# Kernel tuning notes

Hardware: AMD Instinct MI355X
Metric: run time of the kernel (lower is better)

Reference implementation:

```python
import jax, jax.numpy as jnp
import numpy as np

N = 50000        # num_nodes
E = 800000       # num_edges
D_IN = 128
D_OUT = 128
BN_EPS = 1e-5    # torch BatchNorm1d default


def setup_inputs() -> dict:
    key = jax.random.key(0)
    ks = jax.random.split(key, 6)
    x = jax.random.normal(ks[0], (N, D_IN), dtype=jnp.float32)
    edge_index = jax.random.randint(ks[1], (2, E), 0, N, dtype=jnp.int64)
    eps = jnp.zeros((1,), dtype=jnp.float32)  # nn.Parameter(torch.tensor([0.0]))
    lim1 = 1.0 / np.sqrt(D_IN)
    lim2 = 1.0 / np.sqrt(D_OUT)
    W1 = jax.random.uniform(ks[2], (D_OUT, D_IN), jnp.float32, -lim1, lim1)
    b1 = jax.random.uniform(ks[3], (D_OUT,), jnp.float32, -lim1, lim1)
    W2 = jax.random.uniform(ks[4], (D_OUT, D_OUT), jnp.float32, -lim2, lim2)
    b2 = jax.random.uniform(ks[5], (D_OUT,), jnp.float32, -lim2, lim2)
    gamma1 = jnp.ones((D_OUT,), jnp.float32)
    beta1 = jnp.zeros((D_OUT,), jnp.float32)
    gamma2 = jnp.ones((D_OUT,), jnp.float32)
    beta2 = jnp.zeros((D_OUT,), jnp.float32)
    return {"x": x, "edge_index": edge_index, "eps": eps,
            "W1": W1, "b1": b1, "gamma1": gamma1, "beta1": beta1,
            "W2": W2, "b2": b2, "gamma2": gamma2, "beta2": beta2}


def _batch_norm(h, gamma, beta):
    # training-mode BatchNorm1d: biased batch variance, eps=1e-5
    mu = h.mean(axis=0)
    var = h.var(axis=0)
    return gamma * (h - mu) * jax.lax.rsqrt(var + BN_EPS) + beta


def reference(x, edge_index, eps, W1, b1, gamma1, beta1, W2, b2, gamma2, beta2):
    row, col = edge_index[0], edge_index[1]
    # agg[v] = sum_{(v,u) in edges} x[u]   (gather + scatter-add)
    agg = jax.ops.segment_sum(x[col], row, num_segments=N)  # [N, D_IN]
    out = (1.0 + eps) * x + agg                              # [N, D_IN]
    h = jax.nn.relu(_batch_norm(out @ W1.T + b1, gamma1, beta1))
    h = jax.nn.relu(_batch_norm(h @ W2.T + b2, gamma2, beta2))
    return h
```

## Files before the change

### kernel.cpp

```cpp
#include <hip/hip_runtime.h>

#define NN 50000
#define EE 800000
#define DD 128
#define BN_EPS 1e-5f
#define XCONV_B 3125
#define BIN_BLOCKS 200
#define BIN_EDGES 4000
#define NBUCK 1563
#define BCAP 1024
#define NREP 32
#define GEMM_B 782
#define LDA 136

typedef __attribute__((ext_vector_type(8))) short bf16x8;
typedef __attribute__((ext_vector_type(4))) float f32x4;
typedef __attribute__((ext_vector_type(8))) unsigned short u16x8;

__device__ inline unsigned short f2bf(float f) {
  unsigned int u = __float_as_uint(f);
  u = (u + 0x7fffu + ((u >> 16) & 1u)) >> 16;
  return (unsigned short)u;
}
__device__ inline float bf2f(unsigned short b) {
  return __uint_as_float(((unsigned int)b) << 16);
}


__global__ __launch_bounds__(256) void k_prep(const float* __restrict__ x,
                                              const float* __restrict__ W1,
                                              const float* __restrict__ W2,
                                              unsigned short* __restrict__ xb,
                                              unsigned short* __restrict__ W1b,
                                              unsigned short* __restrict__ W2b,
                                              int* __restrict__ bcur,
                                              float* __restrict__ reps) {
  const int b = blockIdx.x;
  const int t = threadIdx.x;
  if (b < XCONV_B) {
    const int gid = b * 256 + t;
    const float4 v0 = ((const float4*)x)[gid * 2];
    const float4 v1 = ((const float4*)x)[gid * 2 + 1];
    ushort4 o0, o1;
    o0.x = f2bf(v0.x); o0.y = f2bf(v0.y); o0.z = f2bf(v0.z); o0.w = f2bf(v0.w);
    o1.x = f2bf(v1.x); o1.y = f2bf(v1.y); o1.z = f2bf(v1.z); o1.w = f2bf(v1.w);
    ((ushort4*)xb)[gid * 2] = o0;
    ((ushort4*)xb)[gid * 2 + 1] = o1;
    if (gid < NBUCK) bcur[gid] = 0;
    if (gid < 4 * NREP * DD) reps[gid] = 0.0f;
  } else if (b < XCONV_B + 16) {
    const int gid = (b - XCONV_B) * 256 + t;
    const float4 v = ((const float4*)W1)[gid];
    ushort4 o;
    o.x = f2bf(v.x); o.y = f2bf(v.y); o.z = f2bf(v.z); o.w = f2bf(v.w);
    ((ushort4*)W1b)[gid] = o;
  } else {
    const int gid = (b - XCONV_B - 16) * 256 + t;
    const float4 v = ((const float4*)W2)[gid];
    ushort4 o;
    o.x = f2bf(v.x); o.y = f2bf(v.y); o.z = f2bf(v.z); o.w = f2bf(v.w);
    ((ushort4*)W2b)[gid] = o;
  }
}

__global__ __launch_bounds__(256) void k_bin0(const int* __restrict__ rows,
                                              const int* __restrict__ cols,
                                              int* __restrict__ bcur,
                                              unsigned int* __restrict__ bbuf) {
  __shared__ int hist[NBUCK];
  __shared__ int lbase[NBUCK];
  const int t = threadIdx.x;
  for (int i = t; i < NBUCK; i += 256) hist[i] = 0;
  __syncthreads();
  const int e0 = blockIdx.x * BIN_EDGES;
  int er[16], ec[16];
#pragma unroll
  for (int i = 0; i < 16; ++i) {
    const int idx = t + i * 256;
    if (idx < BIN_EDGES) {
      er[i] = rows[e0 + idx];
      ec[i] = cols[e0 + idx];
      atomicAdd(&hist[er[i] >> 5], 1);
    }
  }
  __syncthreads();
  for (int i = t; i < NBUCK; i += 256) {
    const int c = hist[i];
    lbase[i] = (c > 0) ? atomicAdd(&bcur[i], c) : 0;
    hist[i] = 0;
  }
  __syncthreads();
#pragma unroll
  for (int i = 0; i < 16; ++i) {
    const int idx = t + i * 256;
    if (idx < BIN_EDGES) {
      const int bk = er[i] >> 5;
      const int lp = lbase[bk] + atomicAdd(&hist[bk], 1);
      if (lp < BCAP)
        bbuf[(size_t)bk * BCAP + lp] =
            ((unsigned)(er[i] & 31) << 16) | (unsigned)ec[i];
    }
  }
}

__global__ __launch_bounds__(128) void k_aggemm1(
    const unsigned short* __restrict__ xb, const float* __restrict__ eps,
    const int* __restrict__ bcnt, const unsigned int* __restrict__ bbuf,
    const unsigned short* __restrict__ W, const float* __restrict__ bias,
    unsigned short* __restrict__ outb, float* __restrict__ sum1r,
    float* __restrict__ sumsq1r) {
  __shared__ unsigned short scols[BCAP];
  __shared__ unsigned short sA[32 * LDA];
  __shared__ int rcnt[32];
  __shared__ int roff[33];
  __shared__ int sscan[128];
  __shared__ float bsum[DD];
  __shared__ float bsq[DD];
  const int t = threadIdx.x;
  const int bk = blockIdx.x;
  const int wv = t >> 6;
  const int lane = t & 63;
  const int sub = lane >> 4;
  const int l16 = lane & 15;

  int n = bcnt[bk];
  n = n < BCAP ? n : BCAP;
  if (t < 32) rcnt[t] = 0;
  bsum[t] = 0.f;
  bsq[t] = 0.f;
  __syncthreads();

  unsigned int ent[8];
  int nl = 0;
  for (int i = t; i < n; i += 128) {
    const unsigned int e = bbuf[(size_t)bk * BCAP + i];
    ent[nl++] = e;
    atomicAdd(&rcnt[e >> 16], 1);
  }
  __syncthreads();
  sscan[t] = (t < 32) ? rcnt[t] : 0;
  __syncthreads();
#pragma unroll
  for (int off = 1; off < 32; off <<= 1) {
    const int v = (t >= off) ? sscan[t - off] : 0;
    __syncthreads();
    sscan[t] += v;
    __syncthreads();
  }
  if (t < 32) {
    roff[t] = sscan[t] - rcnt[t];
    rcnt[t] = 0;
  }
  if (t == 31) roff[32] = sscan[31];
  __syncthreads();
  for (int i = 0; i < nl; ++i) {
    const int r = ent[i] >> 16;
    const int pos = roff[r] + atomicAdd(&rcnt[r], 1);
    scols[pos] = (unsigned short)(ent[i] & 0xffffu);
  }
  __syncthreads();

  {
    const float s = 1.0f + eps[0];
    for (int r = wv; r < 32; r += 2) {
      const int v = bk * 32 + r;
      float acc[8];
#pragma unroll
      for (int j = 0; j < 8; ++j) acc[j] = 0.f;
      if (v < NN) {
        if (sub == 0) {
          const u16x8 a = *(const u16x8*)(xb + (size_t)v * DD + l16 * 8);
#pragma unroll
          for (int j = 0; j < 8; ++j) acc[j] = s * bf2f(a[j]);
        }
        const int beg = roff[r];
        const int end = roff[r + 1];
        int i = beg + sub;
        for (; i + 12 < end; i += 16) {
          const int u0 = scols[i];
          const int u1 = scols[i + 4];
          const int u2 = scols[i + 8];
          const int u3 = scols[i + 12];
          const u16x8 a = *(const u16x8*)(xb + (size_t)u0 * DD + l16 * 8);
          const u16x8 b = *(const u16x8*)(xb + (size_t)u1 * DD + l16 * 8);
          const u16x8 c = *(const u16x8*)(xb + (size_t)u2 * DD + l16 * 8);
          const u16x8 d = *(const u16x8*)(xb + (size_t)u3 * DD + l16 * 8);
#pragma unroll
          for (int j = 0; j < 8; ++j)
            acc[j] += (bf2f(a[j]) + bf2f(b[j])) + (bf2f(c[j]) + bf2f(d[j]));
        }
        for (; i + 4 < end; i += 8) {
          const int u0 = scols[i];
          const int u1 = scols[i + 4];
          const u16x8 a = *(const u16x8*)(xb + (size_t)u0 * DD + l16 * 8);
          const u16x8 b = *(const u16x8*)(xb + (size_t)u1 * DD + l16 * 8);
#pragma unroll
          for (int j = 0; j < 8; ++j) acc[j] += bf2f(a[j]) + bf2f(b[j]);
        }
        if (i < end) {
          const int u = scols[i];
          const u16x8 a = *(const u16x8*)(xb + (size_t)u * DD + l16 * 8);
#pragma unroll
          for (int j = 0; j < 8; ++j) acc[j] += bf2f(a[j]);
        }
      }
#pragma unroll
      for (int j = 0; j < 8; ++j) {
        acc[j] += __shfl_xor(acc[j], 16);
        acc[j] += __shfl_xor(acc[j], 32);
      }
      if (sub == 0) {
        u16x8 o;
#pragma unroll
        for (int j = 0; j < 8; ++j) o[j] = f2bf(acc[j]);
        *(u16x8*)(&sA[r * LDA + l16 * 8]) = o;
      }
    }
  }
  __syncthreads();

  f32x4 acc[8];
#pragma unroll
  for (int nn = 0; nn < 8; ++nn) acc[nn] = (f32x4){0.f, 0.f, 0.f, 0.f};
#pragma unroll
  for (int kk = 0; kk < 4; ++kk) {
    const bf16x8 af =
        *(const bf16x8*)(&sA[(wv * 16 + l16) * LDA + kk * 32 + sub * 8]);
#pragma unroll
    for (int nn = 0; nn < 8; ++nn) {
      const bf16x8 bf =
          *(const bf16x8*)(W + (size_t)(nn * 16 + l16) * DD + sub * 8 + kk * 32);
      acc[nn] = __builtin_amdgcn_mfma_f32_16x16x32_bf16(af, bf, acc[nn], 0, 0, 0);
    }
  }
  const int orow0 = bk * 32 + wv * 16 + sub * 4;
#pragma unroll
  for (int nn = 0; nn < 8; ++nn) {
    const int col = nn * 16 + l16;
    const float bv = bias[col];
    float sv = 0.f, qv = 0.f;
#pragma unroll
    for (int r = 0; r < 4; ++r) {
      const int row = orow0 + r;
      if (row < NN) {
        const float o = acc[nn][r] + bv;
        outb[(size_t)row * DD + col] = f2bf(o);
        sv += o; qv += o * o;
      }
    }
    sv += __shfl_xor(sv, 16); qv += __shfl_xor(qv, 16);
    sv += __shfl_xor(sv, 32); qv += __shfl_xor(qv, 32);
    if (sub == 0) { atomicAdd(&bsum[col], sv); atomicAdd(&bsq[col], qv); }
  }
  __syncthreads();
  {
    const int rep = (bk & (NREP - 1)) * DD;
    atomicAdd(&sum1r[rep + t], bsum[t]);
    atomicAdd(&sumsq1r[rep + t], bsq[t]);
  }
}

__global__ __launch_bounds__(256) void k_gemm2(const unsigned short* __restrict__ A,
                                               const float* __restrict__ sum1r,
                                               const float* __restrict__ sumsq1r,
                                               const float* __restrict__ gamma,
                                               const float* __restrict__ beta,
                                               const unsigned short* __restrict__ W,
                                               const float* __restrict__ bias,
                                               unsigned short* __restrict__ outb,
                                               float* __restrict__ sum2r,
                                               float* __restrict__ sumsq2r) {
  __shared__ float lsc[DD];
  __shared__ float lsh[DD];
  __shared__ float bsum[DD];
  __shared__ float bsq[DD];
  const int tid = threadIdx.x;
  const int wv = tid >> 6;
  const int lane = tid & 63;
  const int quad = lane >> 4;
  const int l16 = lane & 15;
  if (tid < DD) {
    float sm = 0.f, qm = 0.f;
#pragma unroll
    for (int r = 0; r < NREP; ++r) {
      sm += sum1r[r * DD + tid];
      qm += sumsq1r[r * DD + tid];
    }
    const float inv_n = 1.0f / (float)NN;
    const float mean = sm * inv_n;
    const float var = qm * inv_n - mean * mean;
    const float s = gamma[tid] * rsqrtf(var + BN_EPS);
    lsc[tid] = s;
    lsh[tid] = beta[tid] - mean * s;
    bsum[tid] = 0.f;
    bsq[tid] = 0.f;
  }
  __syncthreads();

  const int rowbase = blockIdx.x * 64 + wv * 16 + l16;
  const int arow = rowbase < NN ? rowbase : NN - 1;
  const unsigned short* aptr = A + (size_t)arow * DD + quad * 8;

  f32x4 acc[8];
#pragma unroll
  for (int n = 0; n < 8; ++n) acc[n] = (f32x4){0.f, 0.f, 0.f, 0.f};
#pragma unroll
  for (int kk = 0; kk < 4; ++kk) {
    const int kbase = kk * 32 + quad * 8;
    const u16x8 a = *(const u16x8*)(aptr + kk * 32);
    const float4 s0 = *(const float4*)&lsc[kbase];
    const float4 s1 = *(const float4*)&lsc[kbase + 4];
    const float4 h0 = *(const float4*)&lsh[kbase];
    const float4 h1 = *(const float4*)&lsh[kbase + 4];
    bf16x8 af;
    af[0] = (short)f2bf(fmaxf(fmaf(s0.x, bf2f(a[0]), h0.x), 0.f));
    af[1] = (short)f2bf(fmaxf(fmaf(s0.y, bf2f(a[1]), h0.y), 0.f));
    af[2] = (short)f2bf(fmaxf(fmaf(s0.z, bf2f(a[2]), h0.z), 0.f));
    af[3] = (short)f2bf(fmaxf(fmaf(s0.w, bf2f(a[3]), h0.w), 0.f));
    af[4] = (short)f2bf(fmaxf(fmaf(s1.x, bf2f(a[4]), h1.x), 0.f));
    af[5] = (short)f2bf(fmaxf(fmaf(s1.y, bf2f(a[5]), h1.y), 0.f));
    af[6] = (short)f2bf(fmaxf(fmaf(s1.z, bf2f(a[6]), h1.z), 0.f));
    af[7] = (short)f2bf(fmaxf(fmaf(s1.w, bf2f(a[7]), h1.w), 0.f));
#pragma unroll
    for (int n = 0; n < 8; ++n) {
      const bf16x8 bf =
          *(const bf16x8*)(W + (size_t)(n * 16 + l16) * DD + kbase);
      acc[n] = __builtin_amdgcn_mfma_f32_16x16x32_bf16(af, bf, acc[n], 0, 0, 0);
    }
  }
  const int orow0 = blockIdx.x * 64 + wv * 16 + quad * 4;
#pragma unroll
  for (int n = 0; n < 8; ++n) {
    const int col = n * 16 + l16;
    const float bv = bias[col];
    float sv = 0.f, qv = 0.f;
#pragma unroll
    for (int r = 0; r < 4; ++r) {
      const int row = orow0 + r;
      if (row < NN) {
        const float o = acc[n][r] + bv;
        outb[(size_t)row * DD + col] = f2bf(o);
        sv += o; qv += o * o;
      }
    }
    sv += __shfl_xor(sv, 16); qv += __shfl_xor(qv, 16);
    sv += __shfl_xor(sv, 32); qv += __shfl_xor(qv, 32);
    if (quad == 0) { atomicAdd(&bsum[col], sv); atomicAdd(&bsq[col], qv); }
  }
  __syncthreads();
  if (tid < DD) {
    const int rep = (blockIdx.x & (NREP - 1)) * DD;
    atomicAdd(&sum2r[rep + tid], bsum[tid]);
    atomicAdd(&sumsq2r[rep + tid], bsq[tid]);
  }
}

__global__ void k_bnstats2(const float* __restrict__ sum2r,
                           const float* __restrict__ sumsq2r,
                           const float* __restrict__ gamma,
                           const float* __restrict__ beta,
                           float* __restrict__ scale,
                           float* __restrict__ shift) {
  const int c = threadIdx.x;
  float sm = 0.f, qm = 0.f;
#pragma unroll
  for (int r = 0; r < NREP; ++r) {
    sm += sum2r[r * DD + c];
    qm += sumsq2r[r * DD + c];
  }
  const float inv_n = 1.0f / (float)NN;
  const float mean = sm * inv_n;
  const float var = qm * inv_n - mean * mean;
  const float sc = gamma[c] * rsqrtf(var + BN_EPS);
  scale[c] = sc;
  shift[c] = beta[c] - mean * sc;
}

__global__ __launch_bounds__(256) void k_bnrelu(const unsigned short* __restrict__ in,
                                                const float* __restrict__ scale,
                                                const float* __restrict__ shift,
                                                float* __restrict__ out) {
  __shared__ float lsc[DD];
  __shared__ float lsh[DD];
  const int t = threadIdx.x;
  if (t < DD) {
    lsc[t] = scale[t];
    lsh[t] = shift[t];
  }
  __syncthreads();
  const int gid = blockIdx.x * 256 + t;
  const int c = (gid & 15) * 8;
  const u16x8 a = ((const u16x8*)in)[gid];
  const float4 sc0 = *(const float4*)&lsc[c];
  const float4 sc1 = *(const float4*)&lsc[c + 4];
  const float4 sh0 = *(const float4*)&lsh[c];
  const float4 sh1 = *(const float4*)&lsh[c + 4];
  float4 o0, o1;
  o0.x = fmaxf(fmaf(sc0.x, bf2f(a[0]), sh0.x), 0.f);
  o0.y = fmaxf(fmaf(sc0.y, bf2f(a[1]), sh0.y), 0.f);
  o0.z = fmaxf(fmaf(sc0.z, bf2f(a[2]), sh0.z), 0.f);
  o0.w = fmaxf(fmaf(sc0.w, bf2f(a[3]), sh0.w), 0.f);
  o1.x = fmaxf(fmaf(sc1.x, bf2f(a[4]), sh1.x), 0.f);
  o1.y = fmaxf(fmaf(sc1.y, bf2f(a[5]), sh1.y), 0.f);
  o1.z = fmaxf(fmaf(sc1.z, bf2f(a[6]), sh1.z), 0.f);
  o1.w = fmaxf(fmaf(sc1.w, bf2f(a[7]), sh1.w), 0.f);
  ((float4*)out)[gid * 2] = o0;
  ((float4*)out)[gid * 2 + 1] = o1;
}

extern "C" void kernel_launch(void* const* d_in, const int* in_sizes, int n_in,
                              void* d_out, int out_size, void* d_ws, size_t ws_size,
                              hipStream_t stream) {
  const float* x = (const float*)d_in[0];
  const int* ei = (const int*)d_in[1];
  const float* eps = (const float*)d_in[2];
  const float* W1 = (const float*)d_in[3];
  const float* b1 = (const float*)d_in[4];
  const float* g1 = (const float*)d_in[5];
  const float* be1 = (const float*)d_in[6];
  const float* W2 = (const float*)d_in[7];
  const float* b2 = (const float*)d_in[8];
  const float* g2 = (const float*)d_in[9];
  const float* be2 = (const float*)d_in[10];
  float* out = (float*)d_out;

  const int* rows = ei;
  const int* cols = ei + EE;

  int* bcur = (int*)d_out;
  unsigned short* xb = (unsigned short*)d_out + 2000000;
  unsigned int* bbuf = (unsigned int*)((char*)d_out + 16800000);
  unsigned short* W1b = (unsigned short*)d_out + 11640000;
  unsigned short* W2b = (unsigned short*)d_out + 11680000;
  float* reps = (float*)d_out + 5875000;
  float* sum1r = reps;
  float* sumsq1r = reps + NREP * DD;
  float* sum2r = reps + 2 * NREP * DD;
  float* sumsq2r = reps + 3 * NREP * DD;

  unsigned short* h1b = (unsigned short*)d_ws;
  unsigned short* h2b = h1b + (size_t)NN * DD;
  float* stats = (float*)(h1b + (size_t)2 * NN * DD);
  float* scale2 = stats + 0;
  float* shift2 = stats + 128;

  k_prep<<<XCONV_B + 32, 256, 0, stream>>>(x, W1, W2, xb, W1b, W2b, bcur, reps);
  k_bin0<<<BIN_BLOCKS, 256, 0, stream>>>(rows, cols, bcur, bbuf);
  k_aggemm1<<<NBUCK, 128, 0, stream>>>(xb, eps, bcur, bbuf, W1b, b1, h1b,
                                       sum1r, sumsq1r);
  k_gemm2<<<GEMM_B, 256, 0, stream>>>(h1b, sum1r, sumsq1r, g1, be1, W2b, b2,
                                      h2b, sum2r, sumsq2r);
  k_bnstats2<<<1, 128, 0, stream>>>(sum2r, sumsq2r, g2, be2, scale2, shift2);
  k_bnrelu<<<(NN * DD / 8) / 256, 256, 0, stream>>>(h2b, scale2, shift2, out);
}
```

Before: 202.4 us.

## Widen aggregation-GEMM blocks to four waves and fold BN2 stats into gemm2

The fused aggregate+GEMM1 kernel now runs 256 threads (four waves) per bucket. Rows are split across four waves and the MFMA tile across a 2x2 wave grid, and the 32-entry prefix scan becomes a wave shuffle scan instead of a multi-barrier shared-memory scan. The separate single-block BN2 statistics kernel is removed: the last gemm2 block, found through an atomic done counter zeroed in prep, reduces the replicated sums and writes scale and shift. This saves one kernel launch and raises per-block parallelism, at the cost of extra fences and a last-block serialization tail.

```diff
diff --git a/kernel.cpp b/kernel.cpp
--- a/kernel.cpp
+++ b/kernel.cpp
@@ -46,7 +46,7 @@
     o1.x = f2bf(v1.x); o1.y = f2bf(v1.y); o1.z = f2bf(v1.z); o1.w = f2bf(v1.w);
     ((ushort4*)xb)[gid * 2] = o0;
     ((ushort4*)xb)[gid * 2 + 1] = o1;
-    if (gid < NBUCK) bcur[gid] = 0;
+    if (gid <= NBUCK) bcur[gid] = 0;
     if (gid < 4 * NREP * DD) reps[gid] = 0.0f;
   } else if (b < XCONV_B + 16) {
     const int gid = (b - XCONV_B) * 256 + t;
@@ -103,7 +103,7 @@
   }
 }
 
-__global__ __launch_bounds__(128) void k_aggemm1(
+__global__ __launch_bounds__(256) void k_aggemm1(
     const unsigned short* __restrict__ xb, const float* __restrict__ eps,
     const int* __restrict__ bcnt, const unsigned int* __restrict__ bbuf,
     const unsigned short* __restrict__ W, const float* __restrict__ bias,
@@ -113,7 +113,6 @@
   __shared__ unsigned short sA[32 * LDA];
   __shared__ int rcnt[32];
   __shared__ int roff[33];
-  __shared__ int sscan[128];
   __shared__ float bsum[DD];
   __shared__ float bsq[DD];
   const int t = threadIdx.x;
@@ -126,32 +125,28 @@
   int n = bcnt[bk];
   n = n < BCAP ? n : BCAP;
   if (t < 32) rcnt[t] = 0;
-  bsum[t] = 0.f;
-  bsq[t] = 0.f;
-  __syncthreads();
-
-  unsigned int ent[8];
+  if (t < DD) { bsum[t] = 0.f; bsq[t] = 0.f; }
+  __syncthreads();
+
+  unsigned int ent[4];
   int nl = 0;
-  for (int i = t; i < n; i += 128) {
+  for (int i = t; i < n; i += 256) {
     const unsigned int e = bbuf[(size_t)bk * BCAP + i];
     ent[nl++] = e;
     atomicAdd(&rcnt[e >> 16], 1);
   }
   __syncthreads();
-  sscan[t] = (t < 32) ? rcnt[t] : 0;
-  __syncthreads();
-#pragma unroll
-  for (int off = 1; off < 32; off <<= 1) {
-    const int v = (t >= off) ? sscan[t - off] : 0;
-    __syncthreads();
-    sscan[t] += v;
-    __syncthreads();
-  }
-  if (t < 32) {
-    roff[t] = sscan[t] - rcnt[t];
-    rcnt[t] = 0;
-  }
-  if (t == 31) roff[32] = sscan[31];
+  if (t < 64) {
+    int v = (t < 32) ? rcnt[t] : 0;
+#pragma unroll
+    for (int off = 1; off < 32; off <<= 1) {
+      const int u = __shfl_up(v, off);
+      if (lane >= off) v += u;
+    }
+    if (t < 32) roff[t] = v - rcnt[t];
+    if (t == 31) roff[32] = v;
+    if (t < 32) rcnt[t] = 0;
+  }
   __syncthreads();
   for (int i = 0; i < nl; ++i) {
     const int r = ent[i] >> 16;
@@ -162,7 +157,7 @@
 
   {
     const float s = 1.0f + eps[0];
-    for (int r = wv; r < 32; r += 2) {
+    for (int r = wv; r < 32; r += 4) {
       const int v = bk * 32 + r;
       float acc[8];
 #pragma unroll
@@ -219,24 +214,26 @@
   }
   __syncthreads();
 
-  f32x4 acc[8];
-#pragma unroll
-  for (int nn = 0; nn < 8; ++nn) acc[nn] = (f32x4){0.f, 0.f, 0.f, 0.f};
+  const int wr = wv & 1;
+  const int wc = wv >> 1;
+  f32x4 acc[4];
+#pragma unroll
+  for (int nn = 0; nn < 4; ++nn) acc[nn] = (f32x4){0.f, 0.f, 0.f, 0.f};
 #pragma unroll
   for (int kk = 0; kk < 4; ++kk) {
     const bf16x8 af =
-        *(const bf16x8*)(&sA[(wv * 16 + l16) * LDA + kk * 32 + sub * 8]);
-#pragma unroll
-    for (int nn = 0; nn < 8; ++nn) {
-      const bf16x8 bf =
-          *(const bf16x8*)(W + (size_t)(nn * 16 + l16) * DD + sub * 8 + kk * 32);
+        *(const bf16x8*)(&sA[(wr * 16 + l16) * LDA + kk * 32 + sub * 8]);
+#pragma unroll
+    for (int nn = 0; nn < 4; ++nn) {
+      const bf16x8 bf = *(const bf16x8*)(
+          W + (size_t)(wc * 64 + nn * 16 + l16) * DD + sub * 8 + kk * 32);
       acc[nn] = __builtin_amdgcn_mfma_f32_16x16x32_bf16(af, bf, acc[nn], 0, 0, 0);
     }
   }
-  const int orow0 = bk * 32 + wv * 16 + sub * 4;
-#pragma unroll
-  for (int nn = 0; nn < 8; ++nn) {
-    const int col = nn * 16 + l16;
+  const int orow0 = bk * 32 + wr * 16 + sub * 4;
+#pragma unroll
+  for (int nn = 0; nn < 4; ++nn) {
+    const int col = wc * 64 + nn * 16 + l16;
     const float bv = bias[col];
     float sv = 0.f, qv = 0.f;
 #pragma unroll
@@ -253,7 +250,7 @@
     if (sub == 0) { atomicAdd(&bsum[col], sv); atomicAdd(&bsq[col], qv); }
   }
   __syncthreads();
-  {
+  if (t < DD) {
     const int rep = (bk & (NREP - 1)) * DD;
     atomicAdd(&sum1r[rep + t], bsum[t]);
     atomicAdd(&sumsq1r[rep + t], bsq[t]);
@@ -269,7 +266,12 @@
                                                const float* __restrict__ bias,
                                                unsigned short* __restrict__ outb,
                                                float* __restrict__ sum2r,
-                                               float* __restrict__ sumsq2r) {
+                                               float* __restrict__ sumsq2r,
+                                               const float* __restrict__ gamma2,
+                                               const float* __restrict__ beta2,
+                                               float* __restrict__ scale2,
+                                               float* __restrict__ shift2,
+                                               int* __restrict__ done) {
   __shared__ float lsc[DD];
   __shared__ float lsh[DD];
   __shared__ float bsum[DD];
@@ -353,27 +355,30 @@
     atomicAdd(&sum2r[rep + tid], bsum[tid]);
     atomicAdd(&sumsq2r[rep + tid], bsq[tid]);
   }
-}
-
-__global__ void k_bnstats2(const float* __restrict__ sum2r,
-                           const float* __restrict__ sumsq2r,
-                           const float* __restrict__ gamma,
-                           const float* __restrict__ beta,
-                           float* __restrict__ scale,
-                           float* __restrict__ shift) {
-  const int c = threadIdx.x;
-  float sm = 0.f, qm = 0.f;
-#pragma unroll
-  for (int r = 0; r < NREP; ++r) {
-    sm += sum2r[r * DD + c];
-    qm += sumsq2r[r * DD + c];
-  }
-  const float inv_n = 1.0f / (float)NN;
-  const float mean = sm * inv_n;
-  const float var = qm * inv_n - mean * mean;
-  const float sc = gamma[c] * rsqrtf(var + BN_EPS);
-  scale[c] = sc;
-  shift[c] = beta[c] - mean * sc;
+
+  __threadfence();
+  __shared__ int amlast;
+  if (tid == 0) amlast = (atomicAdd(done, 1) == GEMM_B - 1) ? 1 : 0;
+  __syncthreads();
+  if (amlast) {
+    __threadfence();
+    if (tid < DD) {
+      float sm = 0.f, qm = 0.f;
+#pragma unroll
+      for (int r = 0; r < NREP; ++r) {
+        sm += __hip_atomic_load(&sum2r[r * DD + tid], __ATOMIC_RELAXED,
+                                __HIP_MEMORY_SCOPE_AGENT);
+        qm += __hip_atomic_load(&sumsq2r[r * DD + tid], __ATOMIC_RELAXED,
+                                __HIP_MEMORY_SCOPE_AGENT);
+      }
+      const float inv_n = 1.0f / (float)NN;
+      const float mean = sm * inv_n;
+      const float var = qm * inv_n - mean * mean;
+      const float sc = gamma2[tid] * rsqrtf(var + BN_EPS);
+      scale2[tid] = sc;
+      shift2[tid] = beta2[tid] - mean * sc;
+    }
+  }
 }
 
 __global__ __launch_bounds__(256) void k_bnrelu(const unsigned short* __restrict__ in,
@@ -437,6 +442,7 @@
   float* sumsq1r = reps + NREP * DD;
   float* sum2r = reps + 2 * NREP * DD;
   float* sumsq2r = reps + 3 * NREP * DD;
+  int* done = bcur + NBUCK;
 
   unsigned short* h1b = (unsigned short*)d_ws;
   unsigned short* h2b = h1b + (size_t)NN * DD;
@@ -446,10 +452,10 @@
 
   k_prep<<<XCONV_B + 32, 256, 0, stream>>>(x, W1, W2, xb, W1b, W2b, bcur, reps);
   k_bin0<<<BIN_BLOCKS, 256, 0, stream>>>(rows, cols, bcur, bbuf);
-  k_aggemm1<<<NBUCK, 128, 0, stream>>>(xb, eps, bcur, bbuf, W1b, b1, h1b,
+  k_aggemm1<<<NBUCK, 256, 0, stream>>>(xb, eps, bcur, bbuf, W1b, b1, h1b,
                                        sum1r, sumsq1r);
   k_gemm2<<<GEMM_B, 256, 0, stream>>>(h1b, sum1r, sumsq1r, g1, be1, W2b, b2,
-                                      h2b, sum2r, sumsq2r);
-  k_bnstats2<<<1, 128, 0, stream>>>(sum2r, sumsq2r, g2, be2, scale2, shift2);
+                                      h2b, sum2r, sumsq2r, g2, be2,
+                                      scale2, shift2, done);
   k_bnrelu<<<(NN * DD / 8) / 256, 256, 0, stream>>>(h2b, scale2, shift2, out);
 }
```

Result: slower. 264.6 us (+30.7%).

## Split aggregation by feature quarter and fuse both MLP layers with grid-wide barriers

Applied to the files above, without the earlier changes.

Stores x in bf16 as four 32-column planes and runs aggregation as four passes, one per plane, over 16-row buckets. Each pass gathers narrower rows, which improves cache locality for the random neighbour gathers. Both GEMMs, both batch-norm statistic reductions and the final BN+ReLU move into one persistent kernel of 391 blocks. That kernel uses last-block election plus spin-wait barriers on global flags, which removes the h1/h2 round trips and three kernel launches. The cost is that it only works if all blocks are co-resident, and the aggregated result now makes an extra trip through memory.

```diff
diff --git a/kernel.cpp b/kernel.cpp
--- a/kernel.cpp
+++ b/kernel.cpp
@@ -7,10 +7,11 @@
 #define XCONV_B 3125
 #define BIN_BLOCKS 200
 #define BIN_EDGES 4000
-#define NBUCK 1563
-#define BCAP 1024
+#define NBUCK 3125
+#define BROWS 16
+#define BCAP 512
 #define NREP 32
-#define GEMM_B 782
+#define MLP_B 391
 #define LDA 136
 
 typedef __attribute__((ext_vector_type(8))) short bf16x8;
@@ -25,16 +26,23 @@
 __device__ inline float bf2f(unsigned short b) {
   return __uint_as_float(((unsigned int)b) << 16);
 }
+__device__ inline float ldw(const float* p) {
+  return __hip_atomic_load(p, __ATOMIC_RELAXED, __HIP_MEMORY_SCOPE_AGENT);
+}
+__device__ inline void stw(float* p, float v) {
+  __hip_atomic_store(p, v, __ATOMIC_RELAXED, __HIP_MEMORY_SCOPE_AGENT);
+}
 
 
 __global__ __launch_bounds__(256) void k_prep(const float* __restrict__ x,
                                               const float* __restrict__ W1,
                                               const float* __restrict__ W2,
-                                              unsigned short* __restrict__ xb,
+                                              unsigned short* __restrict__ xq,
                                               unsigned short* __restrict__ W1b,
                                               unsigned short* __restrict__ W2b,
                                               int* __restrict__ bcur,
-                                              float* __restrict__ reps) {
+                                              float* __restrict__ reps,
+                                              int* __restrict__ syncw) {
   const int b = blockIdx.x;
   const int t = threadIdx.x;
   if (b < XCONV_B) {
@@ -44,10 +52,14 @@
     ushort4 o0, o1;
     o0.x = f2bf(v0.x); o0.y = f2bf(v0.y); o0.z = f2bf(v0.z); o0.w = f2bf(v0.w);
     o1.x = f2bf(v1.x); o1.y = f2bf(v1.y); o1.z = f2bf(v1.z); o1.w = f2bf(v1.w);
-    ((ushort4*)xb)[gid * 2] = o0;
-    ((ushort4*)xb)[gid * 2 + 1] = o1;
+    const int node = gid >> 4;
+    const int c0 = (gid & 15) * 8;
+    const size_t dst = (size_t)(c0 >> 5) * (NN * 32) + node * 32 + (c0 & 31);
+    *(ushort4*)(xq + dst) = o0;
+    *(ushort4*)(xq + dst + 4) = o1;
     if (gid < NBUCK) bcur[gid] = 0;
     if (gid < 4 * NREP * DD) reps[gid] = 0.0f;
+    if (gid < 4) syncw[gid] = 0;
   } else if (b < XCONV_B + 16) {
     const int gid = (b - XCONV_B) * 256 + t;
     const float4 v = ((const float4*)W1)[gid];
@@ -80,7 +92,7 @@
     if (idx < BIN_EDGES) {
       er[i] = rows[e0 + idx];
       ec[i] = cols[e0 + idx];
-      atomicAdd(&hist[er[i] >> 5], 1);
+      atomicAdd(&hist[er[i] >> 4], 1);
     }
   }
   __syncthreads();
@@ -94,43 +106,33 @@
   for (int i = 0; i < 16; ++i) {
     const int idx = t + i * 256;
     if (idx < BIN_EDGES) {
-      const int bk = er[i] >> 5;
+      const int bk = er[i] >> 4;
       const int lp = lbase[bk] + atomicAdd(&hist[bk], 1);
       if (lp < BCAP)
         bbuf[(size_t)bk * BCAP + lp] =
-            ((unsigned)(er[i] & 31) << 16) | (unsigned)ec[i];
-    }
-  }
-}
-
-__global__ __launch_bounds__(128) void k_aggemm1(
-    const unsigned short* __restrict__ xb, const float* __restrict__ eps,
+            ((unsigned)(er[i] & 15) << 16) | (unsigned)ec[i];
+    }
+  }
+}
+
+__global__ __launch_bounds__(128) void k_agg(
+    const unsigned short* __restrict__ xq, const float* __restrict__ eps,
     const int* __restrict__ bcnt, const unsigned int* __restrict__ bbuf,
-    const unsigned short* __restrict__ W, const float* __restrict__ bias,
-    unsigned short* __restrict__ outb, float* __restrict__ sum1r,
-    float* __restrict__ sumsq1r) {
+    unsigned short* __restrict__ aggb) {
   __shared__ unsigned short scols[BCAP];
-  __shared__ unsigned short sA[32 * LDA];
-  __shared__ int rcnt[32];
-  __shared__ int roff[33];
-  __shared__ int sscan[128];
-  __shared__ float bsum[DD];
-  __shared__ float bsq[DD];
+  __shared__ int rcnt[BROWS];
+  __shared__ int roff[BROWS + 1];
   const int t = threadIdx.x;
-  const int bk = blockIdx.x;
-  const int wv = t >> 6;
-  const int lane = t & 63;
-  const int sub = lane >> 4;
-  const int l16 = lane & 15;
+  const int id = blockIdx.x;
+  const int q = id / NBUCK;
+  const int bk = id - q * NBUCK;
 
   int n = bcnt[bk];
   n = n < BCAP ? n : BCAP;
-  if (t < 32) rcnt[t] = 0;
-  bsum[t] = 0.f;
-  bsq[t] = 0.f;
-  __syncthreads();
-
-  unsigned int ent[8];
+  if (t < BROWS) rcnt[t] = 0;
+  __syncthreads();
+
+  unsigned int ent[4];
   int nl = 0;
   for (int i = t; i < n; i += 128) {
     const unsigned int e = bbuf[(size_t)bk * BCAP + i];
@@ -138,20 +140,17 @@
     atomicAdd(&rcnt[e >> 16], 1);
   }
   __syncthreads();
-  sscan[t] = (t < 32) ? rcnt[t] : 0;
-  __syncthreads();
-#pragma unroll
-  for (int off = 1; off < 32; off <<= 1) {
-    const int v = (t >= off) ? sscan[t - off] : 0;
-    __syncthreads();
-    sscan[t] += v;
-    __syncthreads();
-  }
-  if (t < 32) {
-    roff[t] = sscan[t] - rcnt[t];
+  if (t < BROWS) {
+    int v = rcnt[t];
+#pragma unroll
+    for (int off = 1; off < BROWS; off <<= 1) {
+      const int u = __shfl_up(v, off);
+      if (t >= off) v += u;
+    }
+    roff[t] = v - rcnt[t];
+    if (t == BROWS - 1) roff[BROWS] = v;
     rcnt[t] = 0;
   }
-  if (t == 31) roff[32] = sscan[31];
   __syncthreads();
   for (int i = 0; i < nl; ++i) {
     const int r = ent[i] >> 16;
@@ -160,252 +159,277 @@
   }
   __syncthreads();
 
-  {
-    const float s = 1.0f + eps[0];
-    for (int r = wv; r < 32; r += 2) {
-      const int v = bk * 32 + r;
-      float acc[8];
-#pragma unroll
-      for (int j = 0; j < 8; ++j) acc[j] = 0.f;
-      if (v < NN) {
-        if (sub == 0) {
-          const u16x8 a = *(const u16x8*)(xb + (size_t)v * DD + l16 * 8);
-#pragma unroll
-          for (int j = 0; j < 8; ++j) acc[j] = s * bf2f(a[j]);
-        }
-        const int beg = roff[r];
-        const int end = roff[r + 1];
-        int i = beg + sub;
-        for (; i + 12 < end; i += 16) {
-          const int u0 = scols[i];
-          const int u1 = scols[i + 4];
-          const int u2 = scols[i + 8];
-          const int u3 = scols[i + 12];
-          const u16x8 a = *(const u16x8*)(xb + (size_t)u0 * DD + l16 * 8);
-          const u16x8 b = *(const u16x8*)(xb + (size_t)u1 * DD + l16 * 8);
-          const u16x8 c = *(const u16x8*)(xb + (size_t)u2 * DD + l16 * 8);
-          const u16x8 d = *(const u16x8*)(xb + (size_t)u3 * DD + l16 * 8);
-#pragma unroll
-          for (int j = 0; j < 8; ++j)
-            acc[j] += (bf2f(a[j]) + bf2f(b[j])) + (bf2f(c[j]) + bf2f(d[j]));
-        }
-        for (; i + 4 < end; i += 8) {
-          const int u0 = scols[i];
-          const int u1 = scols[i + 4];
-          const u16x8 a = *(const u16x8*)(xb + (size_t)u0 * DD + l16 * 8);
-          const u16x8 b = *(const u16x8*)(xb + (size_t)u1 * DD + l16 * 8);
-#pragma unroll
-          for (int j = 0; j < 8; ++j) acc[j] += bf2f(a[j]) + bf2f(b[j]);
-        }
-        if (i < end) {
-          const int u = scols[i];
-          const u16x8 a = *(const u16x8*)(xb + (size_t)u * DD + l16 * 8);
-#pragma unroll
-          for (int j = 0; j < 8; ++j) acc[j] += bf2f(a[j]);
-        }
-      }
-#pragma unroll
-      for (int j = 0; j < 8; ++j) {
-        acc[j] += __shfl_xor(acc[j], 16);
-        acc[j] += __shfl_xor(acc[j], 32);
-      }
-      if (sub == 0) {
-        u16x8 o;
-#pragma unroll
-        for (int j = 0; j < 8; ++j) o[j] = f2bf(acc[j]);
-        *(u16x8*)(&sA[r * LDA + l16 * 8]) = o;
-      }
-    }
-  }
-  __syncthreads();
-
-  f32x4 acc[8];
-#pragma unroll
-  for (int nn = 0; nn < 8; ++nn) acc[nn] = (f32x4){0.f, 0.f, 0.f, 0.f};
-#pragma unroll
-  for (int kk = 0; kk < 4; ++kk) {
-    const bf16x8 af =
-        *(const bf16x8*)(&sA[(wv * 16 + l16) * LDA + kk * 32 + sub * 8]);
-#pragma unroll
-    for (int nn = 0; nn < 8; ++nn) {
-      const bf16x8 bf =
-          *(const bf16x8*)(W + (size_t)(nn * 16 + l16) * DD + sub * 8 + kk * 32);
-      acc[nn] = __builtin_amdgcn_mfma_f32_16x16x32_bf16(af, bf, acc[nn], 0, 0, 0);
-    }
-  }
-  const int orow0 = bk * 32 + wv * 16 + sub * 4;
-#pragma unroll
-  for (int nn = 0; nn < 8; ++nn) {
-    const int col = nn * 16 + l16;
-    const float bv = bias[col];
-    float sv = 0.f, qv = 0.f;
-#pragma unroll
-    for (int r = 0; r < 4; ++r) {
-      const int row = orow0 + r;
-      if (row < NN) {
-        const float o = acc[nn][r] + bv;
-        outb[(size_t)row * DD + col] = f2bf(o);
-        sv += o; qv += o * o;
-      }
-    }
-    sv += __shfl_xor(sv, 16); qv += __shfl_xor(qv, 16);
-    sv += __shfl_xor(sv, 32); qv += __shfl_xor(qv, 32);
-    if (sub == 0) { atomicAdd(&bsum[col], sv); atomicAdd(&bsq[col], qv); }
-  }
-  __syncthreads();
-  {
-    const int rep = (bk & (NREP - 1)) * DD;
-    atomicAdd(&sum1r[rep + t], bsum[t]);
-    atomicAdd(&sumsq1r[rep + t], bsq[t]);
-  }
-}
-
-__global__ __launch_bounds__(256) void k_gemm2(const unsigned short* __restrict__ A,
-                                               const float* __restrict__ sum1r,
-                                               const float* __restrict__ sumsq1r,
-                                               const float* __restrict__ gamma,
-                                               const float* __restrict__ beta,
-                                               const unsigned short* __restrict__ W,
-                                               const float* __restrict__ bias,
-                                               unsigned short* __restrict__ outb,
-                                               float* __restrict__ sum2r,
-                                               float* __restrict__ sumsq2r) {
+  const int g = t >> 3;
+  const int l8 = t & 3 | ((t & 7) & ~3);
+  const unsigned short* xqq = xq + (size_t)q * (NN * 32);
+  const float s = 1.0f + eps[0];
+  const int v = bk * BROWS + g;
+  const ushort4 sv4 = *(const ushort4*)(xqq + (size_t)v * 32 + (t & 7) * 4);
+  float a0 = s * bf2f(sv4.x);
+  float a1 = s * bf2f(sv4.y);
+  float a2 = s * bf2f(sv4.z);
+  float a3 = s * bf2f(sv4.w);
+  int i = roff[g];
+  const int E = roff[g + 1];
+  const int lo = (t & 7) * 4;
+  for (; i + 3 < E; i += 4) {
+    const int u0 = scols[i], u1 = scols[i + 1];
+    const int u2 = scols[i + 2], u3 = scols[i + 3];
+    const ushort4 p0 = *(const ushort4*)(xqq + (size_t)u0 * 32 + lo);
+    const ushort4 p1 = *(const ushort4*)(xqq + (size_t)u1 * 32 + lo);
+    const ushort4 p2 = *(const ushort4*)(xqq + (size_t)u2 * 32 + lo);
+    const ushort4 p3 = *(const ushort4*)(xqq + (size_t)u3 * 32 + lo);
+    a0 += (bf2f(p0.x) + bf2f(p1.x)) + (bf2f(p2.x) + bf2f(p3.x));
+    a1 += (bf2f(p0.y) + bf2f(p1.y)) + (bf2f(p2.y) + bf2f(p3.y));
+    a2 += (bf2f(p0.z) + bf2f(p1.z)) + (bf2f(p2.z) + bf2f(p3.z));
+    a3 += (bf2f(p0.w) + bf2f(p1.w)) + (bf2f(p2.w) + bf2f(p3.w));
+  }
+  for (; i + 1 < E; i += 2) {
+    const int u0 = scols[i], u1 = scols[i + 1];
+    const ushort4 p0 = *(const ushort4*)(xqq + (size_t)u0 * 32 + lo);
+    const ushort4 p1 = *(const ushort4*)(xqq + (size_t)u1 * 32 + lo);
+    a0 += bf2f(p0.x) + bf2f(p1.x);
+    a1 += bf2f(p0.y) + bf2f(p1.y);
+    a2 += bf2f(p0.z) + bf2f(p1.z);
+    a3 += bf2f(p0.w) + bf2f(p1.w);
+  }
+  if (i < E) {
+    const int u0 = scols[i];
+    const ushort4 p0 = *(const ushort4*)(xqq + (size_t)u0 * 32 + lo);
+    a0 += bf2f(p0.x);
+    a1 += bf2f(p0.y);
+    a2 += bf2f(p0.z);
+    a3 += bf2f(p0.w);
+  }
+  ushort4 o;
+  o.x = f2bf(a0); o.y = f2bf(a1); o.z = f2bf(a2); o.w = f2bf(a3);
+  *(ushort4*)(aggb + (size_t)v * DD + q * 32 + lo) = o;
+}
+
+__global__ __launch_bounds__(256, 2) void k_mlp(
+    const unsigned short* __restrict__ aggb, float* __restrict__ sum1r,
+    float* __restrict__ sumsq1r, const float* __restrict__ g1,
+    const float* __restrict__ be1, const unsigned short* __restrict__ W1b,
+    const float* __restrict__ b1, const unsigned short* __restrict__ W2b,
+    const float* __restrict__ b2, float* __restrict__ sum2r,
+    float* __restrict__ sumsq2r, const float* __restrict__ g2,
+    const float* __restrict__ be2, float* __restrict__ scale1,
+    float* __restrict__ shift1, float* __restrict__ scale2,
+    float* __restrict__ shift2, int* __restrict__ syncw,
+    float* __restrict__ out) {
+  __shared__ unsigned short sT[128 * LDA];
   __shared__ float lsc[DD];
   __shared__ float lsh[DD];
-  __shared__ float bsum[DD];
-  __shared__ float bsq[DD];
+  __shared__ int amlast;
   const int tid = threadIdx.x;
+  const int bk = blockIdx.x;
   const int wv = tid >> 6;
   const int lane = tid & 63;
   const int quad = lane >> 4;
   const int l16 = lane & 15;
+  const int rowq = bk * 128 + wv * 32 + quad * 4;
+
+#pragma unroll
+  for (int it = 0; it < 8; ++it) {
+    const int idx = it * 256 + tid;
+    const int row = idx >> 4, seg = idx & 15;
+    int grow = bk * 128 + row;
+    grow = grow < NN ? grow : NN - 1;
+    *(u16x8*)&sT[row * LDA + seg * 8] =
+        *(const u16x8*)(aggb + (size_t)grow * DD + seg * 8);
+  }
+  __syncthreads();
+
+  f32x4 acc[2][8];
+#pragma unroll
+  for (int m = 0; m < 2; ++m)
+#pragma unroll
+    for (int n = 0; n < 8; ++n) acc[m][n] = (f32x4){0.f, 0.f, 0.f, 0.f};
+#pragma unroll
+  for (int kk = 0; kk < 4; ++kk) {
+    const bf16x8 a0 =
+        *(const bf16x8*)&sT[(wv * 32 + l16) * LDA + kk * 32 + quad * 8];
+    const bf16x8 a1 =
+        *(const bf16x8*)&sT[(wv * 32 + 16 + l16) * LDA + kk * 32 + quad * 8];
+#pragma unroll
+    for (int n = 0; n < 8; ++n) {
+      const bf16x8 bf = *(const bf16x8*)(W1b + (size_t)(n * 16 + l16) * DD +
+                                         kk * 32 + quad * 8);
+      acc[0][n] = __builtin_amdgcn_mfma_f32_16x16x32_bf16(a0, bf, acc[0][n], 0, 0, 0);
+      acc[1][n] = __builtin_amdgcn_mfma_f32_16x16x32_bf16(a1, bf, acc[1][n], 0, 0, 0);
+    }
+  }
+#pragma unroll
+  for (int n = 0; n < 8; ++n) {
+    const int col = n * 16 + l16;
+    const float bv = b1[col];
+    float sv = 0.f, qv = 0.f;
+#pragma unroll
+    for (int m = 0; m < 2; ++m)
+#pragma unroll
+      for (int r = 0; r < 4; ++r) {
+        const float o = acc[m][n][r] + bv;
+        acc[m][n][r] = o;
+        if (rowq + m * 16 + r < NN) { sv += o; qv += o * o; }
+      }
+    sv += __shfl_xor(sv, 16); qv += __shfl_xor(qv, 16);
+    sv += __shfl_xor(sv, 32); qv += __shfl_xor(qv, 32);
+    if (quad == 0) {
+      const int rep = (bk & (NREP - 1)) * DD;
+      atomicAdd(&sum1r[rep + col], sv);
+      atomicAdd(&sumsq1r[rep + col], qv);
+    }
+  }
+  __syncthreads();
+#pragma unroll
+  for (int m = 0; m < 2; ++m)
+#pragma unroll
+    for (int n = 0; n < 8; ++n)
+#pragma unroll
+      for (int r = 0; r < 4; ++r)
+        sT[(wv * 32 + m * 16 + quad * 4 + r) * LDA + n * 16 + l16] =
+            f2bf(acc[m][n][r]);
+
+  if (tid == 0) amlast = (atomicAdd(&syncw[0], 1) == MLP_B - 1) ? 1 : 0;
+  __syncthreads();
+  if (amlast) {
+    if (tid < DD) {
+      float sm = 0.f, qm = 0.f;
+#pragma unroll
+      for (int r = 0; r < NREP; ++r) {
+        sm += ldw(&sum1r[r * DD + tid]);
+        qm += ldw(&sumsq1r[r * DD + tid]);
+      }
+      const float inv_n = 1.0f / (float)NN;
+      const float mean = sm * inv_n;
+      const float var = qm * inv_n - mean * mean;
+      const float sc = g1[tid] * rsqrtf(var + BN_EPS);
+      stw(&scale1[tid], sc);
+      stw(&shift1[tid], be1[tid] - mean * sc);
+    }
+    __syncthreads();
+    if (tid == 0)
+      __hip_atomic_store(&syncw[1], 1, __ATOMIC_RELAXED, __HIP_MEMORY_SCOPE_AGENT);
+  }
+  if (tid == 0) {
+    while (__hip_atomic_load(&syncw[1], __ATOMIC_RELAXED,
+                             __HIP_MEMORY_SCOPE_AGENT) == 0)
+      __builtin_amdgcn_s_sleep(32);
+  }
+  __syncthreads();
   if (tid < DD) {
-    float sm = 0.f, qm = 0.f;
-#pragma unroll
-    for (int r = 0; r < NREP; ++r) {
-      sm += sum1r[r * DD + tid];
-      qm += sumsq1r[r * DD + tid];
-    }
-    const float inv_n = 1.0f / (float)NN;
-    const float mean = sm * inv_n;
-    const float var = qm * inv_n - mean * mean;
-    const float s = gamma[tid] * rsqrtf(var + BN_EPS);
-    lsc[tid] = s;
-    lsh[tid] = beta[tid] - mean * s;
-    bsum[tid] = 0.f;
-    bsq[tid] = 0.f;
-  }
-  __syncthreads();
-
-  const int rowbase = blockIdx.x * 64 + wv * 16 + l16;
-  const int arow = rowbase < NN ? rowbase : NN - 1;
-  const unsigned short* aptr = A + (size_t)arow * DD + quad * 8;
-
-  f32x4 acc[8];
-#pragma unroll
-  for (int n = 0; n < 8; ++n) acc[n] = (f32x4){0.f, 0.f, 0.f, 0.f};
+    lsc[tid] = ldw(&scale1[tid]);
+    lsh[tid] = ldw(&shift1[tid]);
+  }
+  __syncthreads();
+
+  f32x4 acc2[2][8];
+#pragma unroll
+  for (int m = 0; m < 2; ++m)
+#pragma unroll
+    for (int n = 0; n < 8; ++n) acc2[m][n] = (f32x4){0.f, 0.f, 0.f, 0.f};
 #pragma unroll
   for (int kk = 0; kk < 4; ++kk) {
-    const int kbase = kk * 32 + quad * 8;
-    const u16x8 a = *(const u16x8*)(aptr + kk * 32);
-    const float4 s0 = *(const float4*)&lsc[kbase];
-    const float4 s1 = *(const float4*)&lsc[kbase + 4];
-    const float4 h0 = *(const float4*)&lsh[kbase];
-    const float4 h1 = *(const float4*)&lsh[kbase + 4];
-    bf16x8 af;
-    af[0] = (short)f2bf(fmaxf(fmaf(s0.x, bf2f(a[0]), h0.x), 0.f));
-    af[1] = (short)f2bf(fmaxf(fmaf(s0.y, bf2f(a[1]), h0.y), 0.f));
-    af[2] = (short)f2bf(fmaxf(fmaf(s0.z, bf2f(a[2]), h0.z), 0.f));
-    af[3] = (short)f2bf(fmaxf(fmaf(s0.w, bf2f(a[3]), h0.w), 0.f));
-    af[4] = (short)f2bf(fmaxf(fmaf(s1.x, bf2f(a[4]), h1.x), 0.f));
-    af[5] = (short)f2bf(fmaxf(fmaf(s1.y, bf2f(a[5]), h1.y), 0.f));
-    af[6] = (short)f2bf(fmaxf(fmaf(s1.z, bf2f(a[6]), h1.z), 0.f));
-    af[7] = (short)f2bf(fmaxf(fmaf(s1.w, bf2f(a[7]), h1.w), 0.f));
+    const int kb = kk * 32 + quad * 8;
+    const float4 s0 = *(const float4*)&lsc[kb];
+    const float4 s1 = *(const float4*)&lsc[kb + 4];
+    const float4 h0 = *(const float4*)&lsh[kb];
+    const float4 h1v = *(const float4*)&lsh[kb + 4];
+    const u16x8 x0 = *(const u16x8*)&sT[(wv * 32 + l16) * LDA + kb];
+    const u16x8 x1 = *(const u16x8*)&sT[(wv * 32 + 16 + l16) * LDA + kb];
+    bf16x8 af0, af1;
+    af0[0] = (short)f2bf(fmaxf(fmaf(s0.x, bf2f(x0[0]), h0.x), 0.f));
+    af0[1] = (short)f2bf(fmaxf(fmaf(s0.y, bf2f(x0[1]), h0.y), 0.f));
+    af0[2] = (short)f2bf(fmaxf(fmaf(s0.z, bf2f(x0[2]), h0.z), 0.f));
+    af0[3] = (short)f2bf(fmaxf(fmaf(s0.w, bf2f(x0[3]), h0.w), 0.f));
+    af0[4] = (short)f2bf(fmaxf(fmaf(s1.x, bf2f(x0[4]), h1v.x), 0.f));
+    af0[5] = (short)f2bf(fmaxf(fmaf(s1.y, bf2f(x0[5]), h1v.y), 0.f));
+    af0[6] = (short)f2bf(fmaxf(fmaf(s1.z, bf2f(x0[6]), h1v.z), 0.f));
+    af0[7] = (short)f2bf(fmaxf(fmaf(s1.w, bf2f(x0[7]), h1v.w), 0.f));
+    af1[0] = (short)f2bf(fmaxf(fmaf(s0.x, bf2f(x1[0]), h0.x), 0.f));
+    af1[1] = (short)f2bf(fmaxf(fmaf(s0.y, bf2f(x1[1]), h0.y), 0.f));
+    af1[2] = (short)f2bf(fmaxf(fmaf(s0.z, bf2f(x1[2]), h0.z), 0.f));
+    af1[3] = (short)f2bf(fmaxf(fmaf(s0.w, bf2f(x1[3]), h0.w), 0.f));
+    af1[4] = (short)f2bf(fmaxf(fmaf(s1.x, bf2f(x1[4]), h1v.x), 0.f));
+    af1[5] = (short)f2bf(fmaxf(fmaf(s1.y, bf2f(x1[5]), h1v.y), 0.f));
+    af1[6] = (short)f2bf(fmaxf(fmaf(s1.z, bf2f(x1[6]), h1v.z), 0.f));
+    af1[7] = (short)f2bf(fmaxf(fmaf(s1.w, bf2f(x1[7]), h1v.w), 0.f));
 #pragma unroll
     for (int n = 0; n < 8; ++n) {
       const bf16x8 bf =
-          *(const bf16x8*)(W + (size_t)(n * 16 + l16) * DD + kbase);
-      acc[n] = __builtin_amdgcn_mfma_f32_16x16x32_bf16(af, bf, acc[n], 0, 0, 0);
-    }
-  }
-  const int orow0 = blockIdx.x * 64 + wv * 16 + quad * 4;
+          *(const bf16x8*)(W2b + (size_t)(n * 16 + l16) * DD + kb);
+      acc2[0][n] = __builtin_amdgcn_mfma_f32_16x16x32_bf16(af0, bf, acc2[0][n], 0, 0, 0);
+      acc2[1][n] = __builtin_amdgcn_mfma_f32_16x16x32_bf16(af1, bf, acc2[1][n], 0, 0, 0);
+    }
+  }
 #pragma unroll
   for (int n = 0; n < 8; ++n) {
     const int col = n * 16 + l16;
-    const float bv = bias[col];
+    const float bv = b2[col];
     float sv = 0.f, qv = 0.f;
 #pragma unroll
-    for (int r = 0; r < 4; ++r) {
-      const int row = orow0 + r;
-      if (row < NN) {
-        const float o = acc[n][r] + bv;
-        outb[(size_t)row * DD + col] = f2bf(o);
-        sv += o; qv += o * o;
+    for (int m = 0; m < 2; ++m)
+#pragma unroll
+      for (int r = 0; r < 4; ++r) {
+        const float o = acc2[m][n][r] + bv;
+        acc2[m][n][r] = o;
+        if (rowq + m * 16 + r < NN) { sv += o; qv += o * o; }
       }
-    }
     sv += __shfl_xor(sv, 16); qv += __shfl_xor(qv, 16);
     sv += __shfl_xor(sv, 32); qv += __shfl_xor(qv, 32);
-    if (quad == 0) { atomicAdd(&bsum[col], sv); atomicAdd(&bsq[col], qv); }
+    if (quad == 0) {
+      const int rep = (bk & (NREP - 1)) * DD;
+      atomicAdd(&sum2r[rep + col], sv);
+      atomicAdd(&sumsq2r[rep + col], qv);
+    }
+  }
+  __syncthreads();
+  if (tid == 0) amlast = (atomicAdd(&syncw[2], 1) == MLP_B - 1) ? 1 : 0;
+  __syncthreads();
+  if (amlast) {
+    if (tid < DD) {
+      float sm = 0.f, qm = 0.f;
+#pragma unroll
+      for (int r = 0; r < NREP; ++r) {
+        sm += ldw(&sum2r[r * DD + tid]);
+        qm += ldw(&sumsq2r[r * DD + tid]);
+      }
+      const float inv_n = 1.0f / (float)NN;
+      const float mean = sm * inv_n;
+      const float var = qm * inv_n - mean * mean;
+      const float sc = g2[tid] * rsqrtf(var + BN_EPS);
+      stw(&scale2[tid], sc);
+      stw(&shift2[tid], be2[tid] - mean * sc);
+    }
+    __syncthreads();
+    if (tid == 0)
+      __hip_atomic_store(&syncw[3], 1, __ATOMIC_RELAXED, __HIP_MEMORY_SCOPE_AGENT);
+  }
+  if (tid == 0) {
+    while (__hip_atomic_load(&syncw[3], __ATOMIC_RELAXED,
+                             __HIP_MEMORY_SCOPE_AGENT) == 0)
+      __builtin_amdgcn_s_sleep(32);
   }
   __syncthreads();
   if (tid < DD) {
-    const int rep = (blockIdx.x & (NREP - 1)) * DD;
-    atomicAdd(&sum2r[rep + tid], bsum[tid]);
-    atomicAdd(&sumsq2r[rep + tid], bsq[tid]);
-  }
-}
-
-__global__ void k_bnstats2(const float* __restrict__ sum2r,
-                           const float* __restrict__ sumsq2r,
-                           const float* __restrict__ gamma,
-                           const float* __restrict__ beta,
-                           float* __restrict__ scale,
-                           float* __restrict__ shift) {
-  const int c = threadIdx.x;
-  float sm = 0.f, qm = 0.f;
-#pragma unroll
-  for (int r = 0; r < NREP; ++r) {
-    sm += sum2r[r * DD + c];
-    qm += sumsq2r[r * DD + c];
-  }
-  const float inv_n = 1.0f / (float)NN;
-  const float mean = sm * inv_n;
-  const float var = qm * inv_n - mean * mean;
-  const float sc = gamma[c] * rsqrtf(var + BN_EPS);
-  scale[c] = sc;
-  shift[c] = beta[c] - mean * sc;
-}
-
-__global__ __launch_bounds__(256) void k_bnrelu(const unsigned short* __restrict__ in,
-                                                const float* __restrict__ scale,
-                                                const float* __restrict__ shift,
-                                                float* __restrict__ out) {
-  __shared__ float lsc[DD];
-  __shared__ float lsh[DD];
-  const int t = threadIdx.x;
-  if (t < DD) {
-    lsc[t] = scale[t];
-    lsh[t] = shift[t];
-  }
-  __syncthreads();
-  const int gid = blockIdx.x * 256 + t;
-  const int c = (gid & 15) * 8;
-  const u16x8 a = ((const u16x8*)in)[gid];
-  const float4 sc0 = *(const float4*)&lsc[c];
-  const float4 sc1 = *(const float4*)&lsc[c + 4];
-  const float4 sh0 = *(const float4*)&lsh[c];
-  const float4 sh1 = *(const float4*)&lsh[c + 4];
-  float4 o0, o1;
-  o0.x = fmaxf(fmaf(sc0.x, bf2f(a[0]), sh0.x), 0.f);
-  o0.y = fmaxf(fmaf(sc0.y, bf2f(a[1]), sh0.y), 0.f);
-  o0.z = fmaxf(fmaf(sc0.z, bf2f(a[2]), sh0.z), 0.f);
-  o0.w = fmaxf(fmaf(sc0.w, bf2f(a[3]), sh0.w), 0.f);
-  o1.x = fmaxf(fmaf(sc1.x, bf2f(a[4]), sh1.x), 0.f);
-  o1.y = fmaxf(fmaf(sc1.y, bf2f(a[5]), sh1.y), 0.f);
-  o1.z = fmaxf(fmaf(sc1.z, bf2f(a[6]), sh1.z), 0.f);
-  o1.w = fmaxf(fmaf(sc1.w, bf2f(a[7]), sh1.w), 0.f);
-  ((float4*)out)[gid * 2] = o0;
-  ((float4*)out)[gid * 2 + 1] = o1;
+    lsc[tid] = ldw(&scale2[tid]);
+    lsh[tid] = ldw(&shift2[tid]);
+  }
+  __syncthreads();
+#pragma unroll
+  for (int n = 0; n < 8; ++n) {
+    const int col = n * 16 + l16;
+    const float sc = lsc[col];
+    const float sh = lsh[col];
+#pragma unroll
+    for (int m = 0; m < 2; ++m)
+#pragma unroll
+      for (int r = 0; r < 4; ++r) {
+        const int row = rowq + m * 16 + r;
+        if (row < NN)
+          out[(size_t)row * DD + col] = fmaxf(fmaf(sc, acc2[m][n][r], sh), 0.f);
+      }
+  }
 }
 
 extern "C" void kernel_launch(void* const* d_in, const int* in_sizes, int n_in,
@@ -428,7 +452,7 @@
   const int* cols = ei + EE;
 
   int* bcur = (int*)d_out;
-  unsigned short* xb = (unsigned short*)d_out + 2000000;
+  unsigned short* xq = (unsigned short*)d_out + 2000000;
   unsigned int* bbuf = (unsigned int*)((char*)d_out + 16800000);
   unsigned short* W1b = (unsigned short*)d_out + 11640000;
   unsigned short* W2b = (unsigned short*)d_out + 11680000;
@@ -438,18 +462,19 @@
   float* sum2r = reps + 2 * NREP * DD;
   float* sumsq2r = reps + 3 * NREP * DD;
 
-  unsigned short* h1b = (unsigned short*)d_ws;
-  unsigned short* h2b = h1b + (size_t)NN * DD;
-  float* stats = (float*)(h1b + (size_t)2 * NN * DD);
-  float* scale2 = stats + 0;
-  float* shift2 = stats + 128;
-
-  k_prep<<<XCONV_B + 32, 256, 0, stream>>>(x, W1, W2, xb, W1b, W2b, bcur, reps);
+  unsigned short* aggb = (unsigned short*)d_ws;
+  float* stf = (float*)((char*)d_ws + 12800000);
+  float* scale1 = stf + 0;
+  float* shift1 = stf + 128;
+  float* scale2 = stf + 256;
+  float* shift2 = stf + 384;
+  int* syncw = (int*)(stf + 512);
+
+  k_prep<<<XCONV_B + 32, 256, 0, stream>>>(x, W1, W2, xq, W1b, W2b, bcur, reps,
+                                           syncw);
   k_bin0<<<BIN_BLOCKS, 256, 0, stream>>>(rows, cols, bcur, bbuf);
-  k_aggemm1<<<NBUCK, 128, 0, stream>>>(xb, eps, bcur, bbuf, W1b, b1, h1b,
-                                       sum1r, sumsq1r);
-  k_gemm2<<<GEMM_B, 256, 0, stream>>>(h1b, sum1r, sumsq1r, g1, be1, W2b, b2,
-                                      h2b, sum2r, sumsq2r);
-  k_bnstats2<<<1, 128, 0, stream>>>(sum2r, sumsq2r, g2, be2, scale2, shift2);
-  k_bnrelu<<<(NN * DD / 8) / 256, 256, 0, stream>>>(h2b, scale2, shift2, out);
-}
+  k_agg<<<4 * NBUCK, 128, 0, stream>>>(xq, eps, bcur, bbuf, aggb);
+  k_mlp<<<MLP_B, 256, 0, stream>>>(aggb, sum1r, sumsq1r, g1, be1, W1b, b1,
+                                   W2b, b2, sum2r, sumsq2r, g2, be2, scale1,
+                                   shift1, scale2, shift2, syncw, out);
+}
```

New measurement: 204.1 us. About the same (+0.8%).
